# Kernel optimization log

Hardware: AMD Instinct MI355X
Metric: run time of the kernel (lower is better)

The kernel has to match this reference:

```python
import jax, jax.numpy as jnp
import numpy as np

N = 2048        # tokens (batch*seq)
H = 4096        # hidden_size (LLaMA-7B)
I = 11008       # intermediate_size (LLaMA-7B)
QMAX = 127.0    # int8 symmetric quant range


def setup_inputs() -> dict:
    key = jax.random.key(0)
    ks = jax.random.split(key, 6)
    # pre-quantized int8 activations (stored as int32) + per-token dynamic scales
    x_q = jax.random.randint(ks[0], (N, H), -127, 128, dtype=jnp.int32)
    x_scale = jax.random.uniform(ks[1], (N,), dtype=jnp.float32) * 0.01 + 1e-4
    # fused [gate; up] int8 weight [2I, H] with per-output-channel scales
    w_gateup = jax.random.randint(ks[2], (2 * I, H), -127, 128, dtype=jnp.int32)
    w_gateup_scale = jax.random.uniform(ks[3], (2 * I,), dtype=jnp.float32) * 0.005 + 1e-4
    # down_proj int8 weight [H, I] with per-output-channel scales
    w_down = jax.random.randint(ks[4], (H, I), -127, 128, dtype=jnp.int32)
    w_down_scale = jax.random.uniform(ks[5], (H,), dtype=jnp.float32) * 0.005 + 1e-4
    return {"x_q": x_q, "x_scale": x_scale, "w_gateup": w_gateup,
            "w_gateup_scale": w_gateup_scale, "w_down": w_down,
            "w_down_scale": w_down_scale}


def reference(x_q, x_scale, w_gateup, w_gateup_scale, w_down, w_down_scale):
    acc = jnp.matmul(x_q, w_gateup.T)                      # [N, 2I] int32
    gateup = acc.astype(jnp.float32) * x_scale[:, None] * w_gateup_scale[None, :]
    # --- fused silu_and_mul + dynamic per-token requantization ---
    gate, up = jnp.split(gateup, 2, axis=-1)               # each [N, I]
    act = jax.nn.silu(gate) * up                           # [N, I]
    s2 = jnp.max(jnp.abs(act), axis=-1) / QMAX             # [N] dynamic scale
    q2 = jnp.clip(jnp.round(act / s2[:, None]), -QMAX, QMAX)  # requantized int8 (as f32)
    out = jnp.matmul(q2, w_down.T.astype(jnp.float32)) * s2[:, None] * w_down_scale[None, :]
    return out                                             # [N, H]
```

## Files before the change

### kernel.cpp

```cpp
#include <hip/hip_runtime.h>
#include <stdint.h>

typedef int i32x4 __attribute__((ext_vector_type(4)));
typedef unsigned short u16x8 __attribute__((ext_vector_type(8)));

#define N_TOK 2048
#define HID   4096
#define INTER 11008
#define TWOI  22016
#define KS1   64
#define KS2   172

#define GLD16(gp, lp) __builtin_amdgcn_global_load_lds( \
    (const __attribute__((address_space(1))) void*)(gp), \
    (__attribute__((address_space(3))) void*)(lp), 16, 0, 0)
#define BAR() __builtin_amdgcn_s_barrier()
#define WVM(n) asm volatile("s_waitcnt vmcnt(" #n ")" ::: "memory")

__device__ __forceinline__ unsigned short f2bf(float f) {
  uint32_t u = __float_as_uint(f);
  uint32_t r = (u + 0x7fffu + ((u >> 16) & 1u)) >> 16;
  return (unsigned short)r;
}

__global__ __launch_bounds__(256) void pack_panel(
    const int* __restrict__ src, uint8_t* __restrict__ dst, int R, int K)
{
  const int u = blockIdx.x * 256 + threadIdx.x;
  const int upk = R * 4;
  const int t = u / upk;
  const int rem = u - t * upk;
  const int r = rem >> 2;
  const int c0 = ((rem & 3) ^ (r & 3)) << 4;
  const int* s = src + (size_t)r * K + t * 64 + c0;
  i32x4 o;
#pragma unroll
  for (int q = 0; q < 4; ++q) {
    i32x4 w = *reinterpret_cast<const i32x4*>(s + q * 4);
    o[q] = (w[0] & 255) | ((w[1] & 255) << 8) | ((w[2] & 255) << 16)
         | ((w[3] & 255) << 24);
  }
  *reinterpret_cast<i32x4*>(dst + (size_t)u * 16) = o;
}

__global__ __launch_bounds__(1024) void zero_mx(float* __restrict__ mx) {
  const int i = blockIdx.x * 1024 + threadIdx.x;
  if (i < N_TOK) mx[i] = 0.0f;
}

__global__ __launch_bounds__(512, 2) void gemm1_k(
    const uint8_t* __restrict__ x8p, const uint8_t* __restrict__ wgp,
    const float* __restrict__ xs, const float* __restrict__ wgs,
    unsigned short* __restrict__ act, float* __restrict__ mx)
{
  __shared__ uint8_t sm[131072];
  const int tid = threadIdx.x;
  const int lane = tid & 63, wid = tid >> 6;
  const int wgm = wid >> 2, wgn = wid & 3;
  const int r15 = lane & 15;
  const int slotC = (((lane >> 4) ^ (r15 & 3)) << 4);

  const int bid = blockIdx.x;
  const int v = (bid & 7) * 86 + (bid >> 3);
  const int mt = v & 7;
  const int nt = v >> 3;

  const uint8_t* pA  = x8p + (size_t)mt * 256 * 64 + tid * 16;
  const uint8_t* pBg = wgp + (size_t)nt * 128 * 64 + tid * 16;
  const uint8_t* pBu = wgp + ((size_t)INTER + nt * 128) * 64 + tid * 16;

  const int arow = (wgm << 7) + r15;
  const int brow = (wgn << 6) + r15;
  i32x4 acc[8][4] = {};

#define STG1(t, s) do {                                        \
    uint8_t* l = sm + (s) * 32768 + tid * 16;                  \
    const uint8_t* a = pA + (size_t)(t) * 131072;              \
    GLD16(a, l);                                               \
    GLD16(a + 8192, l + 8192);                                 \
    GLD16(pBg + (size_t)(t) * 1409024, l + 16384);             \
    GLD16(pBu + (size_t)(t) * 1409024, l + 24576);             \
  } while (0)

  STG1(0, 0); STG1(1, 1); STG1(2, 2);
  WVM(8); BAR();

  for (int t = 0; t < KS1; ++t) {
    const int rem = KS1 - 1 - t;
    if (rem >= 3) STG1(t + 3, (t + 3) & 3);
    const uint8_t* b = sm + (t & 3) * 32768;
    i32x4 bv[4], av[8];
#pragma unroll
    for (int n = 0; n < 4; ++n)
      bv[n] = *reinterpret_cast<const i32x4*>(
          b + 16384 + (brow + n * 16) * 64 + slotC);
#pragma unroll
    for (int m = 0; m < 8; ++m)
      av[m] = *reinterpret_cast<const i32x4*>(b + (arow + m * 16) * 64 + slotC);
    __builtin_amdgcn_s_setprio(1);
#pragma unroll
    for (int m = 0; m < 8; ++m)
#pragma unroll
      for (int n = 0; n < 4; ++n)
        acc[m][n] = __builtin_amdgcn_mfma_i32_16x16x64_i8(
            av[m], bv[n], acc[m][n], 0, 0, 0);
    __builtin_amdgcn_s_setprio(0);
    if (rem >= 3)      { WVM(8); }
    else if (rem == 2) { WVM(4); }
    else if (rem == 1) { WVM(0); }
    BAR();
  }
#undef STG1

  float* gs = (float*)sm;
  const int rq = (lane >> 4) << 2;
  if (wgn < 2) {
#pragma unroll
    for (int m = 0; m < 8; ++m) {
#pragma unroll
      for (int n = 0; n < 4; ++n) {
        const int coll = (wgn << 6) + n * 16 + r15;
        const float wsc = wgs[nt * 128 + coll];
#pragma unroll
        for (int r = 0; r < 4; ++r) {
          const int rowl = (wgm << 7) + m * 16 + rq + r;
          const float g = (float)acc[m][n][r] * xs[mt * 256 + rowl] * wsc;
          gs[rowl * 128 + (coll ^ (((rowl >> 2) & 1) << 4))] = g;
        }
      }
    }
  }
  __syncthreads();
  if (wgn >= 2) {
#pragma unroll
    for (int m = 0; m < 8; ++m) {
      float am[4] = {0.f, 0.f, 0.f, 0.f};
#pragma unroll
      for (int n = 0; n < 4; ++n) {
        const int cu = ((wgn - 2) << 6) + n * 16 + r15;
        const float wsc = wgs[INTER + nt * 128 + cu];
#pragma unroll
        for (int r = 0; r < 4; ++r) {
          const int rowl = (wgm << 7) + m * 16 + rq + r;
          const int grow = mt * 256 + rowl;
          const float uv = (float)acc[m][n][r] * xs[grow] * wsc;
          const float g = gs[rowl * 128 + (cu ^ (((rowl >> 2) & 1) << 4))];
          const float a = g / (1.f + __expf(-g)) * uv;
          act[(size_t)grow * INTER + nt * 128 + cu] = f2bf(a);
          am[r] = fmaxf(am[r], __builtin_fabsf(a));
        }
      }
#pragma unroll
      for (int r = 0; r < 4; ++r) {
#pragma unroll
        for (int off = 1; off < 16; off <<= 1)
          am[r] = fmaxf(am[r], __shfl_xor(am[r], off, 64));
      }
      if (r15 == 0) {
#pragma unroll
        for (int r = 0; r < 4; ++r)
          atomicMax((int*)&mx[mt * 256 + (wgm << 7) + m * 16 + rq + r],
                    __float_as_int(am[r]));
      }
    }
  }
}

__global__ __launch_bounds__(256) void quant_k(
    const unsigned short* __restrict__ act, const float* __restrict__ mx,
    uint8_t* __restrict__ q2p)
{
  const int u = blockIdx.x * 256 + threadIdx.x;
  const int t = u >> 13;
  const int rem = u & 8191;
  const int r = rem >> 2;
  const int c0 = ((rem & 3) ^ (r & 3)) << 4;
  const unsigned short* ap = act + (size_t)r * INTER + t * 64 + c0;
  const float inv = 127.0f / fmaxf(mx[r], 1e-30f);
  u16x8 a0 = *reinterpret_cast<const u16x8*>(ap);
  u16x8 a1 = *reinterpret_cast<const u16x8*>(ap + 8);
  i32x4 o;
#pragma unroll
  for (int q = 0; q < 4; ++q) {
    uint32_t d = 0;
#pragma unroll
    for (int b = 0; b < 4; ++b) {
      const int j = q * 4 + b;
      uint32_t aB = (j < 8) ? a0[j] : a1[j - 8];
      float af = __uint_as_float(aB << 16);
      float rr = rintf(af * inv);
      rr = fminf(fmaxf(rr, -127.f), 127.f);
      d |= ((uint32_t)((int)rr & 255)) << (8 * b);
    }
    o[q] = (int)d;
  }
  *reinterpret_cast<i32x4*>(q2p + (size_t)u * 16) = o;
}

__global__ __launch_bounds__(512, 2) void gemm2_k(
    const uint8_t* __restrict__ q2p, const uint8_t* __restrict__ wdp,
    const float* __restrict__ mx, const float* __restrict__ wds,
    float* __restrict__ out)
{
  __shared__ uint8_t sm[98304];
  const int tid = threadIdx.x;
  const int lane = tid & 63, wid = tid >> 6;
  const int wgm = wid >> 2, wgn = wid & 3;
  const int r15 = lane & 15;
  const int slotC = (((lane >> 4) ^ (r15 & 3)) << 4);

  const int bid = blockIdx.x;
  const int v = (bid & 7) * 32 + (bid >> 3);
  const int nt = v >> 4, mt = v & 15;

  const uint8_t* pA = q2p + (size_t)mt * 128 * 64 + tid * 16;
  const uint8_t* pB = wdp + (size_t)nt * 256 * 64 + tid * 16;

  const int arow = (wgm << 6) + r15;
  const int brow = (wgn << 6) + r15;
  i32x4 acc[4][4] = {};

#define STG2(t, s) do {                                        \
    uint8_t* l = sm + (s) * 24576 + tid * 16;                  \
    GLD16(pA + (size_t)(t) * 131072, l);                       \
    const uint8_t* bb = pB + (size_t)(t) * 262144;             \
    GLD16(bb, l + 8192);                                       \
    GLD16(bb + 8192, l + 16384);                               \
  } while (0)

  STG2(0, 0); STG2(1, 1); STG2(2, 2);
  WVM(6); BAR();

  for (int t = 0; t < KS2; ++t) {
    const int rem = KS2 - 1 - t;
    if (rem >= 3) STG2(t + 3, (t + 3) & 3);
    const uint8_t* b = sm + (t & 3) * 24576;
    i32x4 bv[4], av[4];
#pragma unroll
    for (int n = 0; n < 4; ++n)
      bv[n] = *reinterpret_cast<const i32x4*>(
          b + 8192 + (brow + n * 16) * 64 + slotC);
#pragma unroll
    for (int m = 0; m < 4; ++m)
      av[m] = *reinterpret_cast<const i32x4*>(b + (arow + m * 16) * 64 + slotC);
    __builtin_amdgcn_s_setprio(1);
#pragma unroll
    for (int m = 0; m < 4; ++m)
#pragma unroll
      for (int n = 0; n < 4; ++n)
        acc[m][n] = __builtin_amdgcn_mfma_i32_16x16x64_i8(
            av[m], bv[n], acc[m][n], 0, 0, 0);
    __builtin_amdgcn_s_setprio(0);
    if (rem >= 3)      { WVM(6); }
    else if (rem == 2) { WVM(3); }
    else if (rem == 1) { WVM(0); }
    BAR();
  }
#undef STG2

  const int rq = (lane >> 4) << 2;
#pragma unroll
  for (int m = 0; m < 4; ++m) {
#pragma unroll
    for (int r = 0; r < 4; ++r) {
      const int rowl = (wgm << 6) + m * 16 + rq + r;
      const int grow = mt * 128 + rowl;
      const float s2 = mx[grow] * (1.0f / 127.0f);
      float* op = out + (size_t)grow * HID + nt * 256 + (wgn << 6) + r15;
      const float* wp = wds + nt * 256 + (wgn << 6) + r15;
#pragma unroll
      for (int n = 0; n < 4; ++n)
        op[n * 16] = (float)acc[m][n][r] * s2 * wp[n * 16];
    }
  }
}

extern "C" void kernel_launch(void* const* d_in, const int* in_sizes, int n_in,
                              void* d_out, int out_size, void* d_ws, size_t ws_size,
                              hipStream_t stream)
{
  const int*   x_q = (const int*)d_in[0];
  const float* xs  = (const float*)d_in[1];
  const int*   wg  = (const int*)d_in[2];
  const float* wgs = (const float*)d_in[3];
  const int*   wd  = (const int*)d_in[4];
  const float* wds = (const float*)d_in[5];
  float* out = (float*)d_out;

  uint8_t* ws = (uint8_t*)d_ws;
  uint8_t* x8p = ws;
  uint8_t* wgp = x8p + 8388608;
  uint8_t* wdp = wgp + 90177536;
  unsigned short* act = (unsigned short*)(wdp + 45088768);
  float* mx = (float*)((uint8_t*)act + 45088768);
  uint8_t* q2p = (uint8_t*)mx + 8192;

  zero_mx<<<2, 1024, 0, stream>>>(mx);
  pack_panel<<<2048, 256, 0, stream>>>(x_q, x8p, N_TOK, HID);
  pack_panel<<<22016, 256, 0, stream>>>(wg, wgp, TWOI, HID);
  pack_panel<<<11008, 256, 0, stream>>>(wd, wdp, HID, INTER);

  gemm1_k<<<688, 512, 0, stream>>>(x8p, wgp, xs, wgs, act, mx);
  quant_k<<<5504, 256, 0, stream>>>(act, mx, q2p);
  gemm2_k<<<256, 512, 0, stream>>>(q2p, wdp, mx, wds, out);
}
```

Baseline: 498.0 us.

## Split GEMM k-step into two barrier phases interleaving LDS reads with MFMA

Both GEMM main loops now run each k-step in two halves. The A fragments are loaded in two groups, and the async global-to-LDS copies for the next stage are split across the halves. The second half's LDS reads and A prefetch are issued after the first MFMA batch, so LDS traffic and global loads overlap with matrix math, and register pressure from holding all A fragments drops. The cost is an extra barrier per iteration plus explicit lgkmcnt waits with sched_barriers, which can serialize the schedule.

```diff
diff --git a/kernel.cpp b/kernel.cpp
--- a/kernel.cpp
+++ b/kernel.cpp
@@ -16,6 +16,8 @@
     (__attribute__((address_space(3))) void*)(lp), 16, 0, 0)
 #define BAR() __builtin_amdgcn_s_barrier()
 #define WVM(n) asm volatile("s_waitcnt vmcnt(" #n ")" ::: "memory")
+#define LGKM0() do { asm volatile("s_waitcnt lgkmcnt(0)" ::: "memory"); \
+                     __builtin_amdgcn_sched_barrier(0); } while (0)
 
 __device__ __forceinline__ unsigned short f2bf(float f) {
   uint32_t u = __float_as_uint(f);
@@ -87,31 +89,55 @@
 
   for (int t = 0; t < KS1; ++t) {
     const int rem = KS1 - 1 - t;
-    if (rem >= 3) STG1(t + 3, (t + 3) & 3);
     const uint8_t* b = sm + (t & 3) * 32768;
-    i32x4 bv[4], av[8];
+    uint8_t* lnx = sm + ((t + 3) & 3) * 32768 + tid * 16;
+    i32x4 bv[4], av[4];
 #pragma unroll
     for (int n = 0; n < 4; ++n)
       bv[n] = *reinterpret_cast<const i32x4*>(
           b + 16384 + (brow + n * 16) * 64 + slotC);
 #pragma unroll
-    for (int m = 0; m < 8; ++m)
+    for (int m = 0; m < 4; ++m)
       av[m] = *reinterpret_cast<const i32x4*>(b + (arow + m * 16) * 64 + slotC);
+    if (rem >= 3) {
+      GLD16(pBg + (size_t)(t + 3) * 1409024, lnx + 16384);
+      GLD16(pBu + (size_t)(t + 3) * 1409024, lnx + 24576);
+    }
+    BAR();
+    LGKM0();
     __builtin_amdgcn_s_setprio(1);
 #pragma unroll
-    for (int m = 0; m < 8; ++m)
+    for (int m = 0; m < 4; ++m)
 #pragma unroll
       for (int n = 0; n < 4; ++n)
         acc[m][n] = __builtin_amdgcn_mfma_i32_16x16x64_i8(
             av[m], bv[n], acc[m][n], 0, 0, 0);
     __builtin_amdgcn_s_setprio(0);
-    if (rem >= 3)      { WVM(8); }
-    else if (rem == 2) { WVM(4); }
-    else if (rem == 1) { WVM(0); }
+#pragma unroll
+    for (int m = 0; m < 4; ++m)
+      av[m] = *reinterpret_cast<const i32x4*>(
+          b + (arow + (m + 4) * 16) * 64 + slotC);
+    if (rem >= 3) {
+      const uint8_t* a = pA + (size_t)(t + 3) * 131072;
+      GLD16(a, lnx);
+      GLD16(a + 8192, lnx + 8192);
+      WVM(8);
+    } else if (rem == 2) { WVM(4); }
+    else if (rem == 1)   { WVM(0); }
     BAR();
+    LGKM0();
+    __builtin_amdgcn_s_setprio(1);
+#pragma unroll
+    for (int m = 0; m < 4; ++m)
+#pragma unroll
+      for (int n = 0; n < 4; ++n)
+        acc[m + 4][n] = __builtin_amdgcn_mfma_i32_16x16x64_i8(
+            av[m], bv[n], acc[m + 4][n], 0, 0, 0);
+    __builtin_amdgcn_s_setprio(0);
   }
 #undef STG1
 
+  __syncthreads();
   float* gs = (float*)sm;
   const int rq = (lane >> 4) << 2;
   if (wgn < 2) {
@@ -233,28 +259,50 @@
 
   for (int t = 0; t < KS2; ++t) {
     const int rem = KS2 - 1 - t;
-    if (rem >= 3) STG2(t + 3, (t + 3) & 3);
     const uint8_t* b = sm + (t & 3) * 24576;
-    i32x4 bv[4], av[4];
+    uint8_t* lnx = sm + ((t + 3) & 3) * 24576 + tid * 16;
+    i32x4 bv[4], av[2];
 #pragma unroll
     for (int n = 0; n < 4; ++n)
       bv[n] = *reinterpret_cast<const i32x4*>(
           b + 8192 + (brow + n * 16) * 64 + slotC);
 #pragma unroll
-    for (int m = 0; m < 4; ++m)
+    for (int m = 0; m < 2; ++m)
       av[m] = *reinterpret_cast<const i32x4*>(b + (arow + m * 16) * 64 + slotC);
+    if (rem >= 3) {
+      const uint8_t* bb = pB + (size_t)(t + 3) * 262144;
+      GLD16(bb, lnx + 8192);
+      GLD16(bb + 8192, lnx + 16384);
+    }
+    BAR();
+    LGKM0();
     __builtin_amdgcn_s_setprio(1);
 #pragma unroll
-    for (int m = 0; m < 4; ++m)
+    for (int m = 0; m < 2; ++m)
 #pragma unroll
       for (int n = 0; n < 4; ++n)
         acc[m][n] = __builtin_amdgcn_mfma_i32_16x16x64_i8(
             av[m], bv[n], acc[m][n], 0, 0, 0);
     __builtin_amdgcn_s_setprio(0);
-    if (rem >= 3)      { WVM(6); }
-    else if (rem == 2) { WVM(3); }
-    else if (rem == 1) { WVM(0); }
+#pragma unroll
+    for (int m = 0; m < 2; ++m)
+      av[m] = *reinterpret_cast<const i32x4*>(
+          b + (arow + (m + 2) * 16) * 64 + slotC);
+    if (rem >= 3) {
+      GLD16(pA + (size_t)(t + 3) * 131072, lnx);
+      WVM(6);
+    } else if (rem == 2) { WVM(3); }
+    else if (rem == 1)   { WVM(0); }
     BAR();
+    LGKM0();
+    __builtin_amdgcn_s_setprio(1);
+#pragma unroll
+    for (int m = 0; m < 2; ++m)
+#pragma unroll
+      for (int n = 0; n < 4; ++n)
+        acc[m + 2][n] = __builtin_amdgcn_mfma_i32_16x16x64_i8(
+            av[m], bv[n], acc[m + 2][n], 0, 0, 0);
+    __builtin_amdgcn_s_setprio(0);
   }
 #undef STG2
 
```

Result: faster. 477.8 us (-4.1%).
